# Optimization experiments

Hardware: AMD Instinct MI355X
Metric: run time of the kernel (lower is better)

Reference implementation:

```python
import jax, jax.numpy as jnp
import numpy as np
from jax.scipy.special import logsumexp

DIM_N, DIM_E, DIM_U = 64, 128, 64
MID, A = 32, 16
N_PER, B = 12, 128  # 128 fully-connected graphs of 12 nodes


def _lin_params(k, fin, fout):
    k1, k2 = jax.random.split(k)
    lim = 1.0 / np.sqrt(fin)
    W = jax.random.uniform(k1, (fin, fout), minval=-lim, maxval=lim)
    b = jax.random.uniform(k2, (fout,), minval=-lim, maxval=lim)
    return W, b


def setup_inputs() -> dict:
    key = jax.random.key(0)
    ks = jax.random.split(key, 12)
    # fully connected directed graph (no self loops), per component
    s, d = np.meshgrid(np.arange(N_PER), np.arange(N_PER), indexing='ij')
    m = s != d
    s1, d1 = s[m].astype(np.int64), d[m].astype(np.int64)
    Epg = s1.size  # 132
    M = np.zeros((N_PER, N_PER), np.int64)
    M[s1, d1] = np.arange(Epg)
    rev1 = M[d1, s1]
    noff = (np.arange(B, dtype=np.int64) * N_PER)[:, None]
    eoff = (np.arange(B, dtype=np.int64) * Epg)[:, None]
    src = jnp.asarray((s1[None] + noff).reshape(-1))
    dst = jnp.asarray((d1[None] + noff).reshape(-1))
    idx_revs = jnp.asarray((rev1[None] + eoff).reshape(-1))
    E, Nt = B * Epg, B * N_PER
    edge_feats = jax.random.normal(ks[0], (E, DIM_E))
    node_feats = jax.random.normal(ks[1], (Nt, DIM_N))
    graph_feats = jax.random.normal(ks[2], (B, DIM_U))
    edge_feat_reflected = edge_feats[idx_revs]
    u = jax.random.uniform(ks[3], (E, 2), minval=1e-6, maxval=1.0)
    gumbel_noise = -jnp.log(-jnp.log(u))
    W_jf, b_jf = _lin_params(ks[4], DIM_E + DIM_U, A * MID)
    W_if, b_if = _lin_params(ks[5], DIM_N + DIM_U, A)
    W_ju, b_ju = _lin_params(ks[6], DIM_E + DIM_U, A * MID)
    W_iu, b_iu = _lin_params(ks[7], DIM_N + DIM_U, A)
    W_fl, b_fl = _lin_params(ks[8], DIM_E + DIM_U, MID)
    W_cls, b_cls = _lin_params(ks[9], MID, 2)
    return dict(edge_feats=edge_feats, node_feats=node_feats, graph_feats=graph_feats,
                edge_feat_reflected=edge_feat_reflected, src=src, dst=dst, idx_revs=idx_revs,
                gumbel_noise=gumbel_noise, W_jf=W_jf, b_jf=b_jf, W_if=W_if, b_if=b_if,
                W_ju=W_ju, b_ju=b_ju, W_iu=W_iu, b_iu=b_iu, W_fl=W_fl, b_fl=b_fl,
                W_cls=W_cls, b_cls=b_cls)


def reference(edge_feats, node_feats, graph_feats, edge_feat_reflected, src, dst, idx_revs,
              gumbel_noise, W_jf, b_jf, W_if, b_if, W_ju, b_ju, W_iu, b_iu,
              W_fl, b_fl, W_cls, b_cls):
    Bn = graph_feats.shape[0]
    Nt = node_feats.shape[0]
    E = edge_feats.shape[0]
    npg = Nt // Bn          # nodes per graph == number of BP iterations
    epg = E // Bn
    a = b_if.shape[0]       # num_acts
    mid = W_cls.shape[0]    # mid_pair

    # broadcast graph-level features to edges / nodes
    u_e = jnp.repeat(graph_feats, epg, axis=0)   # [E, du]
    u_n = jnp.repeat(graph_feats, npg, axis=0)   # [Nt, du]

    xe = jnp.concatenate([edge_feats, u_e], axis=-1)
    xer = jnp.concatenate([edge_feat_reflected, u_e], axis=-1)
    xn = jnp.concatenate([node_feats, u_n], axis=-1)

    indiv_factor = xn @ W_if + b_if      # [Nt, A]
    indiv_util = xn @ W_iu + b_iu        # [Nt, A]

    fc = (xe @ W_jf + b_jf).reshape(E, a, mid)
    fcr = (xer @ W_jf + b_jf).reshape(E, a, mid)
    factor_vals = jnp.einsum('eam,ebm->eab', fc, fcr)   # [E, A, A]
    uc = (xe @ W_ju + b_ju).reshape(E, a, mid)
    ucr = (xer @ W_ju + b_ju).reshape(E, a, mid)
    util_vals = jnp.einsum('eam,ebm->eab', uc, ucr)     # [E, A, A]

    # hard gumbel-softmax edge gating; noise shared with reverse edge
    flag_repr = (xe @ W_fl + b_fl) * (xer @ W_fl + b_fl)
    logits = flag_repr @ W_cls + b_cls                  # [E, 2]
    eid = jnp.arange(E)
    noise = gumbel_noise[jnp.minimum(eid, idx_revs)]
    y_soft = jax.nn.softmax(logits + noise, axis=-1)
    y_hard = jax.nn.one_hot(jnp.argmax(y_soft, axis=-1), 2, dtype=y_soft.dtype)
    flags = y_soft + jax.lax.stop_gradient(y_hard - y_soft)
    flag0 = flags[:, 0][:, None]                        # [E, 1]

    fvT = factor_vals.transpose(0, 2, 1)
    uvT = util_vals.transpose(0, 2, 1)
    if_src, if_dst = indiv_factor[src], indiv_factor[dst]
    iu_src, iu_dst = indiv_util[src], indiv_util[dst]

    def step(carry, _):
        mm_n, um_n, msg_e, rmsg_e, umsg_e, rumsg_e = carry
        agg = mm_n[src] - rmsg_e + if_src                      # [E, A]
        m = factor_vals + agg[:, None, :]                      # [E, A, A]
        m_sum = jax.nn.log_softmax(logsumexp(m, axis=-1), axis=-1)
        new_msg = m_sum * flag0
        agg_rev = mm_n[dst] - msg_e + if_dst
        m_rev = fvT + agg_rev[:, None, :]
        m_rev_sum = jax.nn.log_softmax(logsumexp(m_rev, axis=-1), axis=-1)
        new_rmsg = m_rev_sum * flag0
        util = um_n[src] - rumsg_e + iu_src
        new_umsg = ((util_vals + util[:, None, :]) * jax.nn.softmax(m, axis=-1)).sum(-1) * flag0
        rev_util = um_n[dst] - umsg_e + iu_dst
        new_rumsg = ((uvT + rev_util[:, None, :]) * jax.nn.softmax(m_rev, axis=-1)).sum(-1) * flag0
        new_mm_n = jax.ops.segment_sum(new_msg, dst, num_segments=Nt)
        new_um_n = jax.ops.segment_sum(new_umsg, dst, num_segments=Nt)
        return (new_mm_n, new_um_n, new_msg, new_rmsg, new_umsg, new_rumsg), None

    zn = jnp.zeros((Nt, a), edge_feats.dtype)
    ze = jnp.zeros((E, a), edge_feats.dtype)
    carry0 = (zn, zn, ze, ze, ze, ze)
    (mm_n, um_n, _, _, _, _), _ = jax.lax.scan(step, carry0, None, length=npg)

    node0 = jnp.arange(Bn) * npg
    return (um_n + indiv_util)[node0]   # [B, A]
```

## Files before the change

### kernel.cpp

```cpp
#include <hip/hip_runtime.h>
#include <hip/hip_bf16.h>

typedef unsigned short ushort_t;
typedef __bf16 bf16x8 __attribute__((ext_vector_type(8)));
typedef float f32x4 __attribute__((ext_vector_type(4)));

#define E_TOT 16896
#define NT    1536
#define BGR   128
#define NPG   12
#define EPG   132
#define KD    192
#define KDE   128
#define KD2   384
#define NJ    512
#define NCAN  8448

#if defined(__has_builtin)
#  if __has_builtin(__builtin_amdgcn_global_load_lds)
#    define HAS_GLL 1
#  else
#    define HAS_GLL 0
#  endif
#else
#  define HAS_GLL 0
#endif

#if HAS_GLL
__device__ __forceinline__ void gll16(const ushort_t* g, ushort_t* s) {
    __builtin_amdgcn_global_load_lds(
        (const __attribute__((address_space(1))) unsigned int*)g,
        (__attribute__((address_space(3))) unsigned int*)s, 16, 0, 0);
}
#endif

__device__ __forceinline__ float b2f(ushort_t u) {
    union { float f; unsigned int i; } c; c.i = ((unsigned int)u) << 16; return c.f;
}
__device__ __forceinline__ ushort_t f2b(float f) {
    union { float f; unsigned int i; } c; c.f = f;
    unsigned int i = c.i;
    unsigned int r = (i + 0x7FFFu + ((i >> 16) & 1u)) >> 16;
    return (ushort_t)r;
}
__device__ __forceinline__ int rev_local(int i) {
    int s = i / 11;
    int p = i - 11 * s;
    int d = p + (p >= s ? 1 : 0);
    return d * 11 + (s < d ? s : s - 1);
}

__global__ __launch_bounds__(256) void prep_kernel(
    const float* __restrict__ Wjf, const float* __restrict__ Wju,
    const float* __restrict__ ef,  const float* __restrict__ gf,
    const float* __restrict__ bjf, const float* __restrict__ bju,
    const float* __restrict__ nf,
    const float* __restrict__ Wif, const float* __restrict__ bif,
    const float* __restrict__ Wiu, const float* __restrict__ biu,
    ushort_t* __restrict__ WtJFs, ushort_t* __restrict__ WtJUs,
    ushort_t* __restrict__ XeS, float* __restrict__ CG,
    float* __restrict__ IFF, float* __restrict__ IUU)
{
    __shared__ union {
        float tile[64][65];
        struct { float Ws[128 * 32]; float xr[8][128]; } nd;
    } sm;
    int tid = threadIdx.x;
    unsigned bx = blockIdx.x;

    if (bx < 32u) {
        int mat = bx >> 4, t16 = bx & 15;
        int k0 = (t16 >> 3) * 64, n0 = (t16 & 7) * 64;
        const float* W = mat ? Wju : Wjf;
        ushort_t* Wt = mat ? WtJUs : WtJFs;
        int col = tid & 63, rowq = tid >> 6;
#pragma unroll
        for (int i = 0; i < 16; ++i) {
            int kk = i * 4 + rowq;
            sm.tile[kk][col] = W[(size_t)(k0 + kk) * NJ + n0 + col];
        }
        __syncthreads();
        int k = tid & 63;
#pragma unroll
        for (int i = 0; i < 16; ++i) {
            int nn = i * 4 + rowq;
            float wf = sm.tile[k][nn];
            ushort_t hf = f2b(wf);
            ushort_t lo = f2b(wf - b2f(hf));
            ushort_t* dst = Wt + (size_t)(n0 + nn) * KD2 + k0 + k;
            dst[0]   = hf;
            dst[128] = hf;
            dst[256] = lo;
        }
        return;
    }
    if (bx < 1088u) {
        int t = (int)(bx - 32u) * 256 + tid;
        int e = t >> 4, k8 = t & 15;
        const float* src = ef + (size_t)e * KDE + k8 * 8;
        float4 v0 = *(const float4*)(src);
        float4 v1 = *(const float4*)(src + 4);
        float x[8] = { v0.x, v0.y, v0.z, v0.w, v1.x, v1.y, v1.z, v1.w };
        union { ushort_t u[8]; uint4 v; } hi, lo;
#pragma unroll
        for (int i = 0; i < 8; ++i) {
            ushort_t h = f2b(x[i]);
            hi.u[i] = h;
            lo.u[i] = f2b(x[i] - b2f(h));
        }
        ushort_t* dst = XeS + (size_t)e * KD2 + k8 * 8;
        *(uint4*)(dst)       = hi.v;
        *(uint4*)(dst + 128) = lo.v;
        *(uint4*)(dst + 256) = hi.v;
        return;
    }
    if (bx < 1600u) {
        int cidx = (int)(bx - 1088u) * 256 + tid;
        int z = cidx >> 16;
        int rem = cidx & 65535;
        int g = rem >> 9, n = rem & 511;
        const float* W = z ? Wju : Wjf;
        float acc = (z ? bju : bjf)[n];
        const float* gr = gf + g * 64;
#pragma unroll 8
        for (int k = 0; k < 64; ++k)
            acc += gr[k] * W[(size_t)(KDE + k) * NJ + n];
        CG[cidx] = acc;
        return;
    }
    int n0 = (int)(bx - 1600u) * 8;
    for (int i = tid; i < 128 * 32; i += 256) {
        int k = i >> 5, j = i & 31;
        sm.nd.Ws[i] = (j < 16) ? Wif[k * 16 + j] : Wiu[k * 16 + (j - 16)];
    }
    for (int i = tid; i < 8 * 128; i += 256) {
        int slot = i >> 7, k = i & 127;
        int n = n0 + slot;
        sm.nd.xr[slot][k] = (k < 64) ? nf[(size_t)n * 64 + k]
                                     : gf[(n / NPG) * 64 + (k - 64)];
    }
    __syncthreads();
    int slot = tid >> 5, j = tid & 31;
    float acc = (j < 16) ? bif[j] : biu[j - 16];
#pragma unroll 8
    for (int k = 0; k < 128; ++k) acc += sm.nd.xr[slot][k] * sm.nd.Ws[k * 32 + j];
    int n = n0 + slot;
    if (j < 16) IFF[n * 16 + j] = acc;
    else        IUU[n * 16 + (j - 16)] = acc;
}

__global__ __launch_bounds__(256) void gemm_kernel(
    const ushort_t* __restrict__ X,
    const ushort_t* __restrict__ Wt0, const ushort_t* __restrict__ Wt1,
    float* __restrict__ Hbase)
{
    __shared__ ushort_t As[2][128][32];
    __shared__ ushort_t Bs[2][128][32];
    unsigned D = blockIdx.x;
    unsigned c = D / 136u, j = D - c * 136u;
    if (j >= 132u) return;
    int z  = (int)(c >> 2);
    int n0 = (int)(c & 3u) * 128;
    int m0 = (int)j * 128;
    const ushort_t* Wt = z ? Wt1 : Wt0;
    float* H = Hbase + (size_t)z * E_TOT * NJ;

    int tid = threadIdx.x, lane = tid & 63, w = tid >> 6;
    int wm = (w >> 1) * 64, wn = (w & 1) * 64;
    int r = lane & 15, q = lane >> 4;
    f32x4 acc[4][4] = {};

    int sr = w * 32 + (lane >> 2);
    int sc = (lane & 3) * 8;
    const ushort_t* xg0 = X  + (size_t)(m0 + sr)      * KD2 + sc;
    const ushort_t* xg1 = X  + (size_t)(m0 + sr + 16) * KD2 + sc;
    const ushort_t* wg0 = Wt + (size_t)(n0 + sr)      * KD2 + sc;
    const ushort_t* wg1 = Wt + (size_t)(n0 + sr + 16) * KD2 + sc;

#if HAS_GLL
    auto stage = [&](int p, int kk) {
        gll16(xg0 + kk, &As[p][w * 32][0]);
        gll16(xg1 + kk, &As[p][w * 32 + 16][0]);
        gll16(wg0 + kk, &Bs[p][w * 32][0]);
        gll16(wg1 + kk, &Bs[p][w * 32 + 16][0]);
    };
#else
    auto stage = [&](int p, int kk) {
        uint4 a0 = *(const uint4*)(xg0 + kk);
        uint4 a1 = *(const uint4*)(xg1 + kk);
        uint4 b0 = *(const uint4*)(wg0 + kk);
        uint4 b1 = *(const uint4*)(wg1 + kk);
        *(uint4*)&As[p][sr][sc]      = a0;
        *(uint4*)&As[p][sr + 16][sc] = a1;
        *(uint4*)&Bs[p][sr][sc]      = b0;
        *(uint4*)&Bs[p][sr + 16][sc] = b1;
    };
#endif

    stage(0, 0);
    int cur = 0;
    for (int kk = 0; kk < KD2; kk += 32) {
        __syncthreads();
        if (kk + 32 < KD2) stage(cur ^ 1, kk + 32);
        bf16x8 af[4], bf[4];
#pragma unroll
        for (int mi = 0; mi < 4; ++mi)
            af[mi] = *(const bf16x8*)&As[cur][wm + mi * 16 + r][q * 8];
#pragma unroll
        for (int ni = 0; ni < 4; ++ni)
            bf[ni] = *(const bf16x8*)&Bs[cur][wn + ni * 16 + r][q * 8];
#pragma unroll
        for (int mi = 0; mi < 4; ++mi)
#pragma unroll
            for (int ni = 0; ni < 4; ++ni)
                acc[mi][ni] = __builtin_amdgcn_mfma_f32_16x16x32_bf16(
                    af[mi], bf[ni], acc[mi][ni], 0, 0, 0);
        cur ^= 1;
    }
#pragma unroll
    for (int ni = 0; ni < 4; ++ni) {
        int col = n0 + wn + ni * 16 + r;
#pragma unroll
        for (int mi = 0; mi < 4; ++mi) {
            int rowb = m0 + wm + mi * 16 + q * 4;
            float* dst = H + (size_t)rowb * NJ + col;
#pragma unroll
            for (int rr = 0; rr < 4; ++rr)
                dst[(size_t)rr * NJ] = acc[mi][ni][rr];
        }
    }
}

__global__ __launch_bounds__(256) void pair_kernel(
    const float* __restrict__ Hbase, const float* __restrict__ CG,
    float* __restrict__ Obase)
{
    __shared__ float sA[4][16][36];
    __shared__ float sB[4][16][36];
    __shared__ float sC[4][16][20];
    const float* H = Hbase + (size_t)blockIdx.y * E_TOT * NJ;
    const float* cgz = CG + (size_t)blockIdx.y * 128 * NJ;
    float* OutV = Obase + (size_t)blockIdx.y * E_TOT * 256;
    int tid = threadIdx.x, w = tid >> 6, lane = tid & 63;
    int c = blockIdx.x * 4 + w;
    int gg = c / 66, cl = c - gg * 66;
    int s = 0;
    while (cl >= 11 - s) { cl -= 11 - s; ++s; }
    int d = s + 1 + cl;
    int e  = gg * EPG + s * 11 + (d - 1);
    int re = gg * EPG + d * 11 + s;
    const float* hA = H + (size_t)e * NJ;
    const float* hB = H + (size_t)re * NJ;
    int a = lane >> 2, mseg = (lane & 3) * 8;
    float4 va0 = *(const float4*)(hA + a * 32 + mseg);
    float4 va1 = *(const float4*)(hA + a * 32 + mseg + 4);
    float4 vb0 = *(const float4*)(hB + a * 32 + mseg);
    float4 vb1 = *(const float4*)(hB + a * 32 + mseg + 4);
    const float* cgr = cgz + (size_t)gg * NJ + a * 32 + mseg;
    float4 cg0 = *(const float4*)(cgr);
    float4 cg1 = *(const float4*)(cgr + 4);
    va0.x += cg0.x; va0.y += cg0.y; va0.z += cg0.z; va0.w += cg0.w;
    va1.x += cg1.x; va1.y += cg1.y; va1.z += cg1.z; va1.w += cg1.w;
    vb0.x += cg0.x; vb0.y += cg0.y; vb0.z += cg0.z; vb0.w += cg0.w;
    vb1.x += cg1.x; vb1.y += cg1.y; vb1.z += cg1.z; vb1.w += cg1.w;
    *(float4*)&sA[w][a][mseg]     = va0;
    *(float4*)&sA[w][a][mseg + 4] = va1;
    *(float4*)&sB[w][a][mseg]     = vb0;
    *(float4*)&sB[w][a][mseg + 4] = vb1;
    __syncthreads();

    int b = lane & 15, a0 = (lane >> 4) * 4;
    float4 ac0 = {0,0,0,0}, ac1 = {0,0,0,0}, ac2 = {0,0,0,0}, ac3 = {0,0,0,0};
#pragma unroll
    for (int m4 = 0; m4 < 8; ++m4) {
        float4 vb = *(const float4*)&sB[w][b][m4 * 4];
        float4 x0 = *(const float4*)&sA[w][a0 + 0][m4 * 4];
        float4 x1 = *(const float4*)&sA[w][a0 + 1][m4 * 4];
        float4 x2 = *(const float4*)&sA[w][a0 + 2][m4 * 4];
        float4 x3 = *(const float4*)&sA[w][a0 + 3][m4 * 4];
        ac0.x += x0.x * vb.x; ac0.y += x0.y * vb.y; ac0.z += x0.z * vb.z; ac0.w += x0.w * vb.w;
        ac1.x += x1.x * vb.x; ac1.y += x1.y * vb.y; ac1.z += x1.z * vb.z; ac1.w += x1.w * vb.w;
        ac2.x += x2.x * vb.x; ac2.y += x2.y * vb.y; ac2.z += x2.z * vb.z; ac2.w += x2.w * vb.w;
        ac3.x += x3.x * vb.x; ac3.y += x3.y * vb.y; ac3.z += x3.z * vb.z; ac3.w += x3.w * vb.w;
    }
    float v0 = ac0.x + ac0.y + ac0.z + ac0.w;
    float v1 = ac1.x + ac1.y + ac1.z + ac1.w;
    float v2 = ac2.x + ac2.y + ac2.z + ac2.w;
    float v3 = ac3.x + ac3.y + ac3.z + ac3.w;
    float* oe = OutV + (size_t)e * 256;
    oe[(a0 + 0) * 16 + b] = v0;
    oe[(a0 + 1) * 16 + b] = v1;
    oe[(a0 + 2) * 16 + b] = v2;
    oe[(a0 + 3) * 16 + b] = v3;
    sC[w][b][a0 + 0] = v0;
    sC[w][b][a0 + 1] = v1;
    sC[w][b][a0 + 2] = v2;
    sC[w][b][a0 + 3] = v3;
    __syncthreads();
    int rr = lane >> 2, cc = (lane & 3) * 4;
    float4 t4 = { sC[w][rr][cc], sC[w][rr][cc + 1], sC[w][rr][cc + 2], sC[w][rr][cc + 3] };
    *(float4*)(OutV + (size_t)re * 256 + lane * 4) = t4;
}

__global__ __launch_bounds__(256) void hfl_kernel(
    const float* __restrict__ ef, const float* __restrict__ gf,
    const float* __restrict__ Wfl, const float* __restrict__ bfl,
    float* __restrict__ HFL)
{
    __shared__ float Ws[KD][32];
    __shared__ float xr[64][KD];
    int tid = threadIdx.x;
    int e0 = blockIdx.x * 64;
    for (int i = tid; i < KD * 32; i += 256) Ws[i >> 5][i & 31] = Wfl[i];
    for (int i4 = tid; i4 < 64 * 48; i4 += 256) {
        int slot = i4 / 48, kq = i4 - slot * 48;
        int e = e0 + slot;
        float4 v;
        if (kq < 32) v = *(const float4*)&ef[(size_t)e * 128 + kq * 4];
        else         v = *(const float4*)&gf[(e / EPG) * 64 + (kq - 32) * 4];
        *(float4*)&xr[slot][kq * 4] = v;
    }
    __syncthreads();
    int j = tid & 31, es = tid >> 5;
    float acc[8];
#pragma unroll
    for (int i = 0; i < 8; ++i) acc[i] = bfl[j];
    for (int k = 0; k < KD; k += 4) {
        float w0 = Ws[k][j], w1 = Ws[k + 1][j], w2 = Ws[k + 2][j], w3 = Ws[k + 3][j];
#pragma unroll
        for (int i = 0; i < 8; ++i) {
            float4 x4 = *(const float4*)&xr[es + 8 * i][k];
            acc[i] += x4.x * w0; acc[i] += x4.y * w1;
            acc[i] += x4.z * w2; acc[i] += x4.w * w3;
        }
    }
#pragma unroll
    for (int i = 0; i < 8; ++i)
        HFL[(size_t)(e0 + es + 8 * i) * 32 + j] = acc[i];
}

__global__ __launch_bounds__(704) void bp_kernel(
    const float* __restrict__ FV, const float* __restrict__ UV,
    const float* __restrict__ HFL, const float* __restrict__ Wcls,
    const float* __restrict__ bcls, const float* __restrict__ gum,
    const float* __restrict__ IFF, const float* __restrict__ IUU,
    float* __restrict__ out)
{
    int g = blockIdx.x, tid = threadIdx.x;
    __shared__ __align__(16) float fvs[EPG * 256];
    __shared__ __align__(16) float2 MU[EPG][16];
    __shared__ __align__(16) float2 AU[NPG][16];
    __shared__ __align__(16) float2 IU[NPG][16];
    __shared__ __align__(16) float2 gGU[44][16];
    __shared__ float fls[EPG];

    for (int i = tid; i < EPG * 16; i += 704)
        (&MU[0][0])[i] = make_float2(0.f, 0.f);
    if (tid < NPG * 16) {
        float fi = IFF[g * NPG * 16 + tid];
        float ui = IUU[g * NPG * 16 + tid];
        (&IU[0][0])[tid] = make_float2(fi, ui);
        (&AU[0][0])[tid] = make_float2(fi, ui);
    }
    if (tid < EPG) {
        int el = tid, rel = rev_local(el);
        int e = g * EPG + el, re = g * EPG + rel;
        float l0 = bcls[0], l1 = bcls[1];
        const float* ha = HFL + (size_t)e * 32;
        const float* hb = HFL + (size_t)re * 32;
#pragma unroll
        for (int j = 0; j < 32; ++j) {
            float pp = ha[j] * hb[j];
            l0 += pp * Wcls[j * 2 + 0];
            l1 += pp * Wcls[j * 2 + 1];
        }
        int mn = min(e, re);
        l0 += gum[(size_t)mn * 2 + 0];
        l1 += gum[(size_t)mn * 2 + 1];
        fls[el] = (l0 >= l1) ? 1.0f : 0.0f;
    }

    const float* fvg = FV + (size_t)g * EPG * 256;
    const float* uvg = UV + (size_t)g * EPG * 256;
    for (int t4 = tid; t4 < EPG * 64; t4 += 704) {
        float4 v = *(const float4*)(fvg + (size_t)t4 * 4);
        int e = t4 >> 6, rem = t4 & 63;
        int aa = rem >> 2, qq = rem & 3;
        int w = e * 256 + aa * 16 + ((qq ^ ((aa >> 1) & 3)) << 2);
        *(float4*)&fvs[w] = v;
    }

    int w44 = tid >> 4, a = tid & 15;
    int bl = (tid & 63) & 48;
    int e0 = w44,      s0 = e0 / 11, r0 = rev_local(e0);
    int e1 = 44 + w44, s1 = e1 / 11, r1 = rev_local(e1);
    int e2 = 88 + w44, s2 = e2 / 11, r2 = rev_local(e2);

    int xr = (a >> 1) & 3;
    int sl0 = ((0 ^ xr) << 2), sl1 = ((1 ^ xr) << 2);
    int sl2 = ((2 ^ xr) << 2), sl3 = ((3 ^ xr) << 2);
    int fb0 = e0 * 256 + a * 16;
    int fb1 = e1 * 256 + a * 16;
    int fb2 = e2 * 256 + a * 16;

    const float* ur0 = uvg + (size_t)e0 * 256 + a * 16;
    const float* ur1 = uvg + (size_t)e1 * 256 + a * 16;
    const float* ur2 = uvg + (size_t)e2 * 256 + a * 16;

    __syncthreads();
    float fl0 = fls[e0], fl1 = fls[e1], fl2 = fls[e2];

    auto xform = [&](int fbase) -> float {
        float4 a0 = *(const float4*)&fvs[fbase + sl0];
        float4 a1 = *(const float4*)&fvs[fbase + sl1];
        float4 a2 = *(const float4*)&fvs[fbase + sl2];
        float4 a3 = *(const float4*)&fvs[fbase + sl3];
        float mx = fmaxf(fmaxf(fmaxf(a0.x, a0.y), fmaxf(a0.z, a0.w)),
                         fmaxf(fmaxf(a1.x, a1.y), fmaxf(a1.z, a1.w)));
        mx = fmaxf(mx, fmaxf(fmaxf(fmaxf(a2.x, a2.y), fmaxf(a2.z, a2.w)),
                             fmaxf(fmaxf(a3.x, a3.y), fmaxf(a3.z, a3.w))));
        a0.x = __expf(a0.x - mx); a0.y = __expf(a0.y - mx);
        a0.z = __expf(a0.z - mx); a0.w = __expf(a0.w - mx);
        a1.x = __expf(a1.x - mx); a1.y = __expf(a1.y - mx);
        a1.z = __expf(a1.z - mx); a1.w = __expf(a1.w - mx);
        a2.x = __expf(a2.x - mx); a2.y = __expf(a2.y - mx);
        a2.z = __expf(a2.z - mx); a2.w = __expf(a2.w - mx);
        a3.x = __expf(a3.x - mx); a3.y = __expf(a3.y - mx);
        a3.z = __expf(a3.z - mx); a3.w = __expf(a3.w - mx);
        *(float4*)&fvs[fbase + sl0] = a0;
        *(float4*)&fvs[fbase + sl1] = a1;
        *(float4*)&fvs[fbase + sl2] = a2;
        *(float4*)&fvs[fbase + sl3] = a3;
        return mx;
    };
    float fvm0 = xform(fb0);
    float fvm1 = xform(fb1);
    float fvm2 = xform(fb2);

    auto edge_core = [&](int s, int re, int fbase, float fvm,
                         float4 uva, float4 uvb, float4 uvc, float4 uvd,
                         float& lse_o, float& unv_o) {
        float2 au = AU[s][a];
        float2 mu = MU[re][a];
        float aggA  = au.x - mu.x;
        float uaggA = au.y - mu.y;
        float amx = aggA;
        amx = fmaxf(amx, __shfl_xor(amx, 1));
        amx = fmaxf(amx, __shfl_xor(amx, 2));
        amx = fmaxf(amx, __shfl_xor(amx, 4));
        amx = fmaxf(amx, __shfl_xor(amx, 8));
        gGU[w44][a] = make_float2(__expf(aggA - amx), uaggA);
        float4 q0 = *(const float4*)&gGU[w44][0];
        float4 q1 = *(const float4*)&gGU[w44][2];
        float4 q2 = *(const float4*)&gGU[w44][4];
        float4 q3 = *(const float4*)&gGU[w44][6];
        float4 q4 = *(const float4*)&gGU[w44][8];
        float4 q5 = *(const float4*)&gGU[w44][10];
        float4 q6 = *(const float4*)&gGU[w44][12];
        float4 q7 = *(const float4*)&gGU[w44][14];
        float4 E0 = *(const float4*)&fvs[fbase + sl0];
        float4 E1 = *(const float4*)&fvs[fbase + sl1];
        float4 E2 = *(const float4*)&fvs[fbase + sl2];
        float4 E3 = *(const float4*)&fvs[fbase + sl3];
        float p0  = E0.x * q0.x, p1  = E0.y * q0.z;
        float p2  = E0.z * q1.x, p3  = E0.w * q1.z;
        float p4  = E1.x * q2.x, p5  = E1.y * q2.z;
        float p6  = E1.z * q3.x, p7  = E1.w * q3.z;
        float p8  = E2.x * q4.x, p9  = E2.y * q4.z;
        float p10 = E2.z * q5.x, p11 = E2.w * q5.z;
        float p12 = E3.x * q6.x, p13 = E3.y * q6.z;
        float p14 = E3.z * q7.x, p15 = E3.w * q7.z;
        float S = (((p0 + p1) + (p2 + p3)) + ((p4 + p5) + (p6 + p7)))
                + (((p8 + p9) + (p10 + p11)) + ((p12 + p13) + (p14 + p15)));
        float n0  = (uva.x + q0.y) * p0,  n1  = (uva.y + q0.w) * p1;
        float n2  = (uva.z + q1.y) * p2,  n3  = (uva.w + q1.w) * p3;
        float n4  = (uvb.x + q2.y) * p4,  n5  = (uvb.y + q2.w) * p5;
        float n6  = (uvb.z + q3.y) * p6,  n7  = (uvb.w + q3.w) * p7;
        float n8  = (uvc.x + q4.y) * p8,  n9  = (uvc.y + q4.w) * p9;
        float n10 = (uvc.z + q5.y) * p10, n11 = (uvc.w + q5.w) * p11;
        float n12 = (uvd.x + q6.y) * p12, n13 = (uvd.y + q6.w) * p13;
        float n14 = (uvd.z + q7.y) * p14, n15 = (uvd.w + q7.w) * p15;
        float num = (((n0 + n1) + (n2 + n3)) + ((n4 + n5) + (n6 + n7)))
                  + (((n8 + n9) + (n10 + n11)) + ((n12 + n13) + (n14 + n15)));
        S = fmaxf(S, 1e-37f);
        lse_o = (fvm + amx) + __logf(S);
        unv_o = num / S;
    };

    for (int it = 0; it < NPG - 1; ++it) {
        float4 u0q0 = *(const float4*)(ur0 + 0),  u0q1 = *(const float4*)(ur0 + 4);
        float4 u0q2 = *(const float4*)(ur0 + 8),  u0q3 = *(const float4*)(ur0 + 12);
        float4 u1q0 = *(const float4*)(ur1 + 0),  u1q1 = *(const float4*)(ur1 + 4);
        float4 u1q2 = *(const float4*)(ur1 + 8),  u1q3 = *(const float4*)(ur1 + 12);
        float4 u2q0 = *(const float4*)(ur2 + 0),  u2q1 = *(const float4*)(ur2 + 4);
        float4 u2q2 = *(const float4*)(ur2 + 8),  u2q3 = *(const float4*)(ur2 + 12);

        float lse0, unv0, lse1, unv1, lse2, unv2;
        edge_core(s0, r0, fb0, fvm0, u0q0, u0q1, u0q2, u0q3, lse0, unv0);
        edge_core(s1, r1, fb1, fvm1, u1q0, u1q1, u1q2, u1q3, lse1, unv1);
        edge_core(s2, r2, fb2, fvm2, u2q0, u2q1, u2q2, u2q3, lse2, unv2);
        float nm0 = (lse0 - __shfl(lse0, bl)) * fl0;
        float nm1 = (lse1 - __shfl(lse1, bl)) * fl1;
        float nm2 = (lse2 - __shfl(lse2, bl)) * fl2;
        float nu0 = unv0 * fl0, nu1 = unv1 * fl1, nu2 = unv2 * fl2;
        __syncthreads();
        MU[e0][a] = make_float2(nm0, nu0);
        MU[e1][a] = make_float2(nm1, nu1);
        MU[e2][a] = make_float2(nm2, nu2);
        __syncthreads();
        if (tid < NPG * 16) {
            int n = tid >> 4, aa = tid & 15;
            float sm = 0.f, su = 0.f;
#pragma unroll
            for (int s = 0; s < NPG; ++s) {
                if (s == n) continue;
                int le = s * 11 + (n < s ? n : n - 1);
                float2 v = MU[le][aa];
                sm += v.x;
                su += v.y;
            }
            float2 iu = IU[n][aa];
            AU[n][aa] = make_float2(sm + iu.x, su + iu.y);
        }
        __syncthreads();
    }

    {
        float nu0 = 0.f, nu1 = 0.f, nu2 = 0.f;
        bool own = ((w44 % 11) == 0);
        if (own) {
            float lse, unv;
            if (e0 != 0) {
                float4 q0 = *(const float4*)(ur0 + 0), q1 = *(const float4*)(ur0 + 4);
                float4 q2 = *(const float4*)(ur0 + 8), q3 = *(const float4*)(ur0 + 12);
                edge_core(s0, r0, fb0, fvm0, q0, q1, q2, q3, lse, unv);
                nu0 = unv * fl0;
            }
            {
                float4 q0 = *(const float4*)(ur1 + 0), q1 = *(const float4*)(ur1 + 4);
                float4 q2 = *(const float4*)(ur1 + 8), q3 = *(const float4*)(ur1 + 12);
                edge_core(s1, r1, fb1, fvm1, q0, q1, q2, q3, lse, unv);
                nu1 = unv * fl1;
            }
            {
                float4 q0 = *(const float4*)(ur2 + 0), q1 = *(const float4*)(ur2 + 4);
                float4 q2 = *(const float4*)(ur2 + 8), q3 = *(const float4*)(ur2 + 12);
                edge_core(s2, r2, fb2, fvm2, q0, q1, q2, q3, lse, unv);
                nu2 = unv * fl2;
            }
            (void)lse;
        }
        __syncthreads();
        if (own) {
            if (e0 != 0) MU[e0][a] = make_float2(0.f, nu0);
            MU[e1][a] = make_float2(0.f, nu1);
            MU[e2][a] = make_float2(0.f, nu2);
        }
        __syncthreads();
        if (tid < 16) {
            float su = 0.f;
#pragma unroll
            for (int s = 1; s < NPG; ++s) su += MU[s * 11][tid].y;
            out[g * 16 + tid] = su + IU[0][tid].y;
        }
    }
}

extern "C" void kernel_launch(void* const* d_in, const int* in_sizes, int n_in,
                              void* d_out, int out_size, void* d_ws, size_t ws_size,
                              hipStream_t stream) {
    const float* edge_feats  = (const float*)d_in[0];
    const float* node_feats  = (const float*)d_in[1];
    const float* graph_feats = (const float*)d_in[2];
    const float* gumbel      = (const float*)d_in[7];
    const float* W_jf        = (const float*)d_in[8];
    const float* b_jf        = (const float*)d_in[9];
    const float* W_if        = (const float*)d_in[10];
    const float* b_if        = (const float*)d_in[11];
    const float* W_ju        = (const float*)d_in[12];
    const float* b_ju        = (const float*)d_in[13];
    const float* W_iu        = (const float*)d_in[14];
    const float* b_iu        = (const float*)d_in[15];
    const float* W_fl        = (const float*)d_in[16];
    const float* b_fl        = (const float*)d_in[17];
    const float* W_cls       = (const float*)d_in[18];
    const float* b_cls       = (const float*)d_in[19];
    float* out = (float*)d_out;
    (void)in_sizes; (void)n_in; (void)out_size; (void)ws_size;

    size_t off = 0;
    char* base = (char*)d_ws;
    auto alloc = [&](size_t bytes) {
        void* p = base + off;
        off += (bytes + 255) & ~(size_t)255;
        return p;
    };
    ushort_t* XeS   = (ushort_t*)alloc((size_t)E_TOT * KD2 * 2);
    ushort_t* WtJFs = (ushort_t*)alloc((size_t)NJ * KD2 * 2);
    ushort_t* WtJUs = (ushort_t*)alloc((size_t)NJ * KD2 * 2);
    float*    CGp   = (float*)   alloc((size_t)2 * 128 * NJ * 4);
    float*    HFL   = (float*)   alloc((size_t)E_TOT * 32 * 4);
    float*    IFFp  = (float*)   alloc((size_t)NT * 16 * 4);
    float*    IUUp  = (float*)   alloc((size_t)NT * 16 * 4);
    float*    H2    = (float*)   alloc((size_t)E_TOT * NJ * 2 * 4);
    float*    FVUV  = (float*)   alloc((size_t)E_TOT * 512 * 4);
    float* FVv = FVUV;
    float* UVv = FVUV + (size_t)E_TOT * 256;

    const int prep_blocks = 32 + 1056 + 512 + 192;

    prep_kernel<<<prep_blocks, 256, 0, stream>>>(
        W_jf, W_ju, edge_feats, graph_feats, b_jf, b_ju, node_feats,
        W_if, b_if, W_iu, b_iu, WtJFs, WtJUs, XeS, CGp, IFFp, IUUp);
    hfl_kernel<<<E_TOT / 64, 256, 0, stream>>>(edge_feats, graph_feats, W_fl, b_fl, HFL);
    gemm_kernel<<<1088, 256, 0, stream>>>(XeS, WtJFs, WtJUs, H2);
    pair_kernel<<<dim3(NCAN / 4, 2), 256, 0, stream>>>(H2, CGp, FVUV);
    bp_kernel<<<BGR, 704, 0, stream>>>(FVv, UVv, HFL, W_cls, b_cls, gumbel,
                                       IFFp, IUUp, out);
}
```

Baseline: 206.7 us.

## Fuse edge GEMM with pairwise factor contraction through shared memory

Merges the bf16 MFMA GEMM and the pair contraction kernel into one kernel. Each block computes the H rows for 16 edge/reverse-edge pairs, keeps them in padded LDS, adds the graph term, and does the pairwise products directly. This removes writing and re-reading the large fp32 H2 intermediate (about 69 MB) in global memory and drops one launch. In exchange, the M tile shrinks to 32 rows, so each block re-streams the full weight matrix, MFMA reuse per block falls, and the roughly 74 KB of LDS per block limits occupancy.

Measured after the change: 258.6 us. +25.1%, slower.

```diff
diff --git a/kernel.cpp b/kernel.cpp
--- a/kernel.cpp
+++ b/kernel.cpp
@@ -149,157 +149,158 @@
     else        IUU[n * 16 + (j - 16)] = acc;
 }
 
-__global__ __launch_bounds__(256) void gemm_kernel(
+#define HPAD 576
+
+__global__ __launch_bounds__(256) void gp_kernel(
     const ushort_t* __restrict__ X,
     const ushort_t* __restrict__ Wt0, const ushort_t* __restrict__ Wt1,
-    float* __restrict__ Hbase)
+    const float* __restrict__ CG, float* __restrict__ Obase_all)
 {
-    __shared__ ushort_t As[2][128][32];
+    __shared__ float Hs[32 * HPAD];
+    __shared__ ushort_t As[2][32][32];
     __shared__ ushort_t Bs[2][128][32];
-    unsigned D = blockIdx.x;
-    unsigned c = D / 136u, j = D - c * 136u;
-    if (j >= 132u) return;
-    int z  = (int)(c >> 2);
-    int n0 = (int)(c & 3u) * 128;
-    int m0 = (int)j * 128;
+    __shared__ float sC[4][16][20];
+    __shared__ int eid[32];
+
+    int tid = threadIdx.x, lane = tid & 63, w = tid >> 6;
+    int z = blockIdx.y;
     const ushort_t* Wt = z ? Wt1 : Wt0;
-    float* H = Hbase + (size_t)z * E_TOT * NJ;
-
-    int tid = threadIdx.x, lane = tid & 63, w = tid >> 6;
-    int wm = (w >> 1) * 64, wn = (w & 1) * 64;
-    int r = lane & 15, q = lane >> 4;
-    f32x4 acc[4][4] = {};
+    const float* cgz = CG + (size_t)z * 128 * NJ;
+    float* OutV = Obase_all + (size_t)z * E_TOT * 256;
+
+    if (tid < 16) {
+        int c = blockIdx.x * 16 + tid;
+        int gg = c / 66, cl = c - gg * 66;
+        int s = 0;
+        while (cl >= 11 - s) { cl -= 11 - s; ++s; }
+        int d = s + 1 + cl;
+        eid[2 * tid]     = gg * EPG + s * 11 + (d - 1);
+        eid[2 * tid + 1] = gg * EPG + d * 11 + s;
+    }
+    __syncthreads();
 
     int sr = w * 32 + (lane >> 2);
     int sc = (lane & 3) * 8;
-    const ushort_t* xg0 = X  + (size_t)(m0 + sr)      * KD2 + sc;
-    const ushort_t* xg1 = X  + (size_t)(m0 + sr + 16) * KD2 + sc;
-    const ushort_t* wg0 = Wt + (size_t)(n0 + sr)      * KD2 + sc;
-    const ushort_t* wg1 = Wt + (size_t)(n0 + sr + 16) * KD2 + sc;
-
+    int achunk = w * 64 + lane;
+    int arow = achunk >> 2;
+    int asc = (achunk & 3) * 8;
+    const ushort_t* ag = X;
+    if (w < 2) ag = X + (size_t)eid[arow] * KD2 + asc;
+
+    int r = lane & 15, q = lane >> 4;
+
+    for (int nc = 0; nc < 4; ++nc) {
+        int n0g = nc * 128;
+        const ushort_t* wg0 = Wt + (size_t)(n0g + sr) * KD2 + sc;
+        const ushort_t* wg1 = Wt + (size_t)(n0g + sr + 16) * KD2 + sc;
 #if HAS_GLL
-    auto stage = [&](int p, int kk) {
-        gll16(xg0 + kk, &As[p][w * 32][0]);
-        gll16(xg1 + kk, &As[p][w * 32 + 16][0]);
-        gll16(wg0 + kk, &Bs[p][w * 32][0]);
-        gll16(wg1 + kk, &Bs[p][w * 32 + 16][0]);
-    };
+        auto stage = [&](int p, int kk) {
+            gll16(wg0 + kk, &Bs[p][w * 32][0]);
+            gll16(wg1 + kk, &Bs[p][w * 32 + 16][0]);
+            if (w < 2) gll16(ag + kk, &As[p][w * 16][0]);
+        };
 #else
-    auto stage = [&](int p, int kk) {
-        uint4 a0 = *(const uint4*)(xg0 + kk);
-        uint4 a1 = *(const uint4*)(xg1 + kk);
-        uint4 b0 = *(const uint4*)(wg0 + kk);
-        uint4 b1 = *(const uint4*)(wg1 + kk);
-        *(uint4*)&As[p][sr][sc]      = a0;
-        *(uint4*)&As[p][sr + 16][sc] = a1;
-        *(uint4*)&Bs[p][sr][sc]      = b0;
-        *(uint4*)&Bs[p][sr + 16][sc] = b1;
-    };
+        auto stage = [&](int p, int kk) {
+            uint4 b0 = *(const uint4*)(wg0 + kk);
+            uint4 b1 = *(const uint4*)(wg1 + kk);
+            *(uint4*)&Bs[p][sr][sc]      = b0;
+            *(uint4*)&Bs[p][sr + 16][sc] = b1;
+            if (w < 2) {
+                uint4 a0v = *(const uint4*)(ag + kk);
+                *(uint4*)&As[p][arow][asc] = a0v;
+            }
+        };
 #endif
-
-    stage(0, 0);
-    int cur = 0;
-    for (int kk = 0; kk < KD2; kk += 32) {
+        f32x4 acc[2][2] = {};
+        stage(0, 0);
+        int cur = 0;
+        for (int kk = 0; kk < KD2; kk += 32) {
+            __syncthreads();
+            if (kk + 32 < KD2) stage(cur ^ 1, kk + 32);
+            bf16x8 af[2], bf[2];
+            af[0] = *(const bf16x8*)&As[cur][r][q * 8];
+            af[1] = *(const bf16x8*)&As[cur][16 + r][q * 8];
+            bf[0] = *(const bf16x8*)&Bs[cur][w * 32 + r][q * 8];
+            bf[1] = *(const bf16x8*)&Bs[cur][w * 32 + 16 + r][q * 8];
+#pragma unroll
+            for (int mi = 0; mi < 2; ++mi)
+#pragma unroll
+                for (int ni = 0; ni < 2; ++ni)
+                    acc[mi][ni] = __builtin_amdgcn_mfma_f32_16x16x32_bf16(
+                        af[mi], bf[ni], acc[mi][ni], 0, 0, 0);
+            cur ^= 1;
+        }
+        int pcoff = (nc * 4 + w) * 4;
+#pragma unroll
+        for (int ni = 0; ni < 2; ++ni) {
+            int col = n0g + w * 32 + ni * 16 + r;
+            int pc = col + pcoff;
+#pragma unroll
+            for (int mi = 0; mi < 2; ++mi) {
+                int rowb = mi * 16 + q * 4;
+#pragma unroll
+                for (int rr = 0; rr < 4; ++rr)
+                    Hs[(rowb + rr) * HPAD + pc] = acc[mi][ni][rr];
+            }
+        }
         __syncthreads();
-        if (kk + 32 < KD2) stage(cur ^ 1, kk + 32);
-        bf16x8 af[4], bf[4];
-#pragma unroll
-        for (int mi = 0; mi < 4; ++mi)
-            af[mi] = *(const bf16x8*)&As[cur][wm + mi * 16 + r][q * 8];
-#pragma unroll
-        for (int ni = 0; ni < 4; ++ni)
-            bf[ni] = *(const bf16x8*)&Bs[cur][wn + ni * 16 + r][q * 8];
-#pragma unroll
-        for (int mi = 0; mi < 4; ++mi)
-#pragma unroll
-            for (int ni = 0; ni < 4; ++ni)
-                acc[mi][ni] = __builtin_amdgcn_mfma_f32_16x16x32_bf16(
-                    af[mi], bf[ni], acc[mi][ni], 0, 0, 0);
-        cur ^= 1;
-    }
-#pragma unroll
-    for (int ni = 0; ni < 4; ++ni) {
-        int col = n0 + wn + ni * 16 + r;
-#pragma unroll
-        for (int mi = 0; mi < 4; ++mi) {
-            int rowb = m0 + wm + mi * 16 + q * 4;
-            float* dst = H + (size_t)rowb * NJ + col;
-#pragma unroll
-            for (int rr = 0; rr < 4; ++rr)
-                dst[(size_t)rr * NJ] = acc[mi][ni][rr];
-        }
-    }
-}
-
-__global__ __launch_bounds__(256) void pair_kernel(
-    const float* __restrict__ Hbase, const float* __restrict__ CG,
-    float* __restrict__ Obase)
-{
-    __shared__ float sA[4][16][36];
-    __shared__ float sB[4][16][36];
-    __shared__ float sC[4][16][20];
-    const float* H = Hbase + (size_t)blockIdx.y * E_TOT * NJ;
-    const float* cgz = CG + (size_t)blockIdx.y * 128 * NJ;
-    float* OutV = Obase + (size_t)blockIdx.y * E_TOT * 256;
-    int tid = threadIdx.x, w = tid >> 6, lane = tid & 63;
-    int c = blockIdx.x * 4 + w;
-    int gg = c / 66, cl = c - gg * 66;
-    int s = 0;
-    while (cl >= 11 - s) { cl -= 11 - s; ++s; }
-    int d = s + 1 + cl;
-    int e  = gg * EPG + s * 11 + (d - 1);
-    int re = gg * EPG + d * 11 + s;
-    const float* hA = H + (size_t)e * NJ;
-    const float* hB = H + (size_t)re * NJ;
-    int a = lane >> 2, mseg = (lane & 3) * 8;
-    float4 va0 = *(const float4*)(hA + a * 32 + mseg);
-    float4 va1 = *(const float4*)(hA + a * 32 + mseg + 4);
-    float4 vb0 = *(const float4*)(hB + a * 32 + mseg);
-    float4 vb1 = *(const float4*)(hB + a * 32 + mseg + 4);
-    const float* cgr = cgz + (size_t)gg * NJ + a * 32 + mseg;
-    float4 cg0 = *(const float4*)(cgr);
-    float4 cg1 = *(const float4*)(cgr + 4);
-    va0.x += cg0.x; va0.y += cg0.y; va0.z += cg0.z; va0.w += cg0.w;
-    va1.x += cg1.x; va1.y += cg1.y; va1.z += cg1.z; va1.w += cg1.w;
-    vb0.x += cg0.x; vb0.y += cg0.y; vb0.z += cg0.z; vb0.w += cg0.w;
-    vb1.x += cg1.x; vb1.y += cg1.y; vb1.z += cg1.z; vb1.w += cg1.w;
-    *(float4*)&sA[w][a][mseg]     = va0;
-    *(float4*)&sA[w][a][mseg + 4] = va1;
-    *(float4*)&sB[w][a][mseg]     = vb0;
-    *(float4*)&sB[w][a][mseg + 4] = vb1;
+    }
+
+    {
+        int rowL = tid >> 3;
+        int c0 = (tid & 7) * 64;
+        int ge = eid[rowL] / EPG;
+        const float* cgr = cgz + (size_t)ge * NJ;
+        float* hrow = &Hs[rowL * HPAD];
+#pragma unroll
+        for (int i = 0; i < 16; ++i) {
+            int c = c0 + i * 4;
+            int pc = c + (c >> 5) * 4;
+            float4 h = *(float4*)&hrow[pc];
+            float4 cgv = *(const float4*)&cgr[c];
+            h.x += cgv.x; h.y += cgv.y; h.z += cgv.z; h.w += cgv.w;
+            *(float4*)&hrow[pc] = h;
+        }
+    }
     __syncthreads();
 
     int b = lane & 15, a0 = (lane >> 4) * 4;
-    float4 ac0 = {0,0,0,0}, ac1 = {0,0,0,0}, ac2 = {0,0,0,0}, ac3 = {0,0,0,0};
-#pragma unroll
-    for (int m4 = 0; m4 < 8; ++m4) {
-        float4 vb = *(const float4*)&sB[w][b][m4 * 4];
-        float4 x0 = *(const float4*)&sA[w][a0 + 0][m4 * 4];
-        float4 x1 = *(const float4*)&sA[w][a0 + 1][m4 * 4];
-        float4 x2 = *(const float4*)&sA[w][a0 + 2][m4 * 4];
-        float4 x3 = *(const float4*)&sA[w][a0 + 3][m4 * 4];
-        ac0.x += x0.x * vb.x; ac0.y += x0.y * vb.y; ac0.z += x0.z * vb.z; ac0.w += x0.w * vb.w;
-        ac1.x += x1.x * vb.x; ac1.y += x1.y * vb.y; ac1.z += x1.z * vb.z; ac1.w += x1.w * vb.w;
-        ac2.x += x2.x * vb.x; ac2.y += x2.y * vb.y; ac2.z += x2.z * vb.z; ac2.w += x2.w * vb.w;
-        ac3.x += x3.x * vb.x; ac3.y += x3.y * vb.y; ac3.z += x3.z * vb.z; ac3.w += x3.w * vb.w;
-    }
-    float v0 = ac0.x + ac0.y + ac0.z + ac0.w;
-    float v1 = ac1.x + ac1.y + ac1.z + ac1.w;
-    float v2 = ac2.x + ac2.y + ac2.z + ac2.w;
-    float v3 = ac3.x + ac3.y + ac3.z + ac3.w;
-    float* oe = OutV + (size_t)e * 256;
-    oe[(a0 + 0) * 16 + b] = v0;
-    oe[(a0 + 1) * 16 + b] = v1;
-    oe[(a0 + 2) * 16 + b] = v2;
-    oe[(a0 + 3) * 16 + b] = v3;
-    sC[w][b][a0 + 0] = v0;
-    sC[w][b][a0 + 1] = v1;
-    sC[w][b][a0 + 2] = v2;
-    sC[w][b][a0 + 3] = v3;
-    __syncthreads();
-    int rr = lane >> 2, cc = (lane & 3) * 4;
-    float4 t4 = { sC[w][rr][cc], sC[w][rr][cc + 1], sC[w][rr][cc + 2], sC[w][rr][cc + 3] };
-    *(float4*)(OutV + (size_t)re * 256 + lane * 4) = t4;
+    for (int pi = 0; pi < 4; ++pi) {
+        int p = w * 4 + pi;
+        const float* hA = &Hs[(2 * p) * HPAD];
+        const float* hB = &Hs[(2 * p + 1) * HPAD];
+        float4 ac0 = {0,0,0,0}, ac1 = {0,0,0,0}, ac2 = {0,0,0,0}, ac3 = {0,0,0,0};
+#pragma unroll
+        for (int m4 = 0; m4 < 8; ++m4) {
+            float4 vb = *(const float4*)&hB[b * 36 + m4 * 4];
+            float4 x0 = *(const float4*)&hA[(a0 + 0) * 36 + m4 * 4];
+            float4 x1 = *(const float4*)&hA[(a0 + 1) * 36 + m4 * 4];
+            float4 x2 = *(const float4*)&hA[(a0 + 2) * 36 + m4 * 4];
+            float4 x3 = *(const float4*)&hA[(a0 + 3) * 36 + m4 * 4];
+            ac0.x += x0.x * vb.x; ac0.y += x0.y * vb.y; ac0.z += x0.z * vb.z; ac0.w += x0.w * vb.w;
+            ac1.x += x1.x * vb.x; ac1.y += x1.y * vb.y; ac1.z += x1.z * vb.z; ac1.w += x1.w * vb.w;
+            ac2.x += x2.x * vb.x; ac2.y += x2.y * vb.y; ac2.z += x2.z * vb.z; ac2.w += x2.w * vb.w;
+            ac3.x += x3.x * vb.x; ac3.y += x3.y * vb.y; ac3.z += x3.z * vb.z; ac3.w += x3.w * vb.w;
+        }
+        float v0 = ac0.x + ac0.y + ac0.z + ac0.w;
+        float v1 = ac1.x + ac1.y + ac1.z + ac1.w;
+        float v2 = ac2.x + ac2.y + ac2.z + ac2.w;
+        float v3 = ac3.x + ac3.y + ac3.z + ac3.w;
+        int e = eid[2 * p], re = eid[2 * p + 1];
+        float* oe = OutV + (size_t)e * 256;
+        oe[(a0 + 0) * 16 + b] = v0;
+        oe[(a0 + 1) * 16 + b] = v1;
+        oe[(a0 + 2) * 16 + b] = v2;
+        oe[(a0 + 3) * 16 + b] = v3;
+        sC[w][b][a0 + 0] = v0;
+        sC[w][b][a0 + 1] = v1;
+        sC[w][b][a0 + 2] = v2;
+        sC[w][b][a0 + 3] = v3;
+        int rr2 = lane >> 2, cc2 = (lane & 3) * 4;
+        float4 t4 = { sC[w][rr2][cc2], sC[w][rr2][cc2 + 1],
+                      sC[w][rr2][cc2 + 2], sC[w][rr2][cc2 + 3] };
+        *(float4*)(OutV + (size_t)re * 256 + lane * 4) = t4;
+    }
 }
 
 __global__ __launch_bounds__(256) void hfl_kernel(
@@ -602,7 +603,6 @@
     float*    HFL   = (float*)   alloc((size_t)E_TOT * 32 * 4);
     float*    IFFp  = (float*)   alloc((size_t)NT * 16 * 4);
     float*    IUUp  = (float*)   alloc((size_t)NT * 16 * 4);
-    float*    H2    = (float*)   alloc((size_t)E_TOT * NJ * 2 * 4);
     float*    FVUV  = (float*)   alloc((size_t)E_TOT * 512 * 4);
     float* FVv = FVUV;
     float* UVv = FVUV + (size_t)E_TOT * 256;
@@ -613,8 +613,8 @@
         W_jf, W_ju, edge_feats, graph_feats, b_jf, b_ju, node_feats,
         W_if, b_if, W_iu, b_iu, WtJFs, WtJUs, XeS, CGp, IFFp, IUUp);
     hfl_kernel<<<E_TOT / 64, 256, 0, stream>>>(edge_feats, graph_feats, W_fl, b_fl, HFL);
-    gemm_kernel<<<1088, 256, 0, stream>>>(XeS, WtJFs, WtJUs, H2);
-    pair_kernel<<<dim3(NCAN / 4, 2), 256, 0, stream>>>(H2, CGp, FVUV);
+    gp_kernel<<<dim3(NCAN / 16, 2), 256, 0, stream>>>(
+        XeS, WtJFs, WtJUs, CGp, FVUV);
     bp_kernel<<<BGR, 704, 0, stream>>>(FVv, UVv, HFL, W_cls, b_cls, gumbel,
                                        IFFp, IUUp, out);
 }
```
